# Performance work log

Hardware: AMD Instinct MI355X
Metric: run time of the kernel (lower is better)

The kernel has to match this reference:

```python
import jax, jax.numpy as jnp
import numpy as np

N = 100000
E = 1600000
D = 128  # embedding_dim
H = 128  # hidden_channels


def setup_inputs() -> dict:
    key = jax.random.key(0)
    ks = jax.random.split(key, 8)
    x = jax.random.normal(ks[0], (N, D), dtype=jnp.float32)
    edge_index = jax.random.randint(ks[1], (2, E), 0, N, dtype=jnp.int64)
    s = 1.0 / np.sqrt(D)
    W1l = jax.random.uniform(ks[2], (H, D), minval=-s, maxval=s, dtype=jnp.float32)
    W1r = jax.random.uniform(ks[3], (H, D), minval=-s, maxval=s, dtype=jnp.float32)
    b1 = jnp.zeros((H,), dtype=jnp.float32)
    s2 = 1.0 / np.sqrt(H)
    W2l = jax.random.uniform(ks[4], (H, H), minval=-s2, maxval=s2, dtype=jnp.float32)
    W2r = jax.random.uniform(ks[5], (H, H), minval=-s2, maxval=s2, dtype=jnp.float32)
    b2 = jnp.zeros((H,), dtype=jnp.float32)
    return {"x": x, "edge_index": edge_index, "W1l": W1l, "b1": b1, "W1r": W1r,
            "W2l": W2l, "b2": b2, "W2r": W2r}


def _sage_conv(h, src, dst, Wl, b, Wr, n_nodes):
    # mean aggregation of source-node features onto target nodes
    msg = h[src]                                             # [E, F] gather
    agg = jax.ops.segment_sum(msg, dst, num_segments=n_nodes)  # [N, F]
    deg = jax.ops.segment_sum(jnp.ones((src.shape[0],), h.dtype), dst,
                              num_segments=n_nodes)
    mean = agg / jnp.maximum(deg, 1.0)[:, None]
    return mean @ Wl.T + b + h @ Wr.T                        # lin_l(agg) + lin_r(x)


def reference(x, edge_index, W1l, b1, W1r, W2l, b2, W2r):
    src, dst = edge_index[0], edge_index[1]
    n = x.shape[0]
    x1 = jax.nn.relu(_sage_conv(x, src, dst, W1l, b1, W1r, n))
    x2 = jax.nn.relu(_sage_conv(x1, src, dst, W2l, b2, W2r, n))
    return jnp.concatenate((x1[:, :, None], x2[:, :, None]), axis=2)  # [N, H, 2]
```

## Files before the change

kernel.cpp:

```cpp
#include <hip/hip_runtime.h>

typedef unsigned char u8;
typedef unsigned short u16;
typedef unsigned int u32;
typedef unsigned long long u64;
typedef short bf16x8 __attribute__((ext_vector_type(8)));
typedef float f32x4 __attribute__((ext_vector_type(4)));
typedef float f32x2 __attribute__((ext_vector_type(2)));

#define NSB 32
#define MAXW 26
#define CAPL 513
#define CAPW 3072
#define CAPQ 768
#define G1 512
#define CH2 16

static __device__ __forceinline__ float relu(float v) { return v > 0.f ? v : 0.f; }

static __device__ __forceinline__ u16 f2bf(float f) {
  u32 u = __float_as_uint(f);
  u32 r = (u + 0x7FFF + ((u >> 16) & 1)) >> 16;
  return (u16)r;
}
static __device__ __forceinline__ u32 pack2(float a, float b) {
  return (u32)f2bf(a) | ((u32)f2bf(b) << 16);
}
static __device__ __forceinline__ float bflo(u32 u) { return __uint_as_float(u << 16); }
static __device__ __forceinline__ float bfhi(u32 u) { return __uint_as_float(u & 0xFFFF0000u); }

__global__ __launch_bounds__(256) void k_prep(
    const float* __restrict__ w1l, const float* __restrict__ w1r,
    const float* __restrict__ w2l, const float* __restrict__ w2r,
    u16* __restrict__ bfrag) {
  int i = blockIdx.x * 256 + threadIdx.x;
  int e = i & 7;
  int lane = (i >> 3) & 63;
  int jb = (i >> 9) & 7;
  int ks = (i >> 12) & 7;
  int m = i >> 15;
  int k = ks * 32 + (lane >> 4) * 8 + e;
  int j = jb * 16 + (lane & 15);
  const float* wl = m ? w2l : w1l;
  const float* wr = m ? w2r : w1r;
  float v = (k < 128) ? wl[j * 128 + k] : wr[j * 128 + (k - 128)];
  bfrag[i] = f2bf(v);
}

__global__ __launch_bounds__(256) void k_f2b(const float* __restrict__ x,
                                             u16* __restrict__ xb,
                                             u8* __restrict__ x8, int total8) {
  int i = blockIdx.x * 256 + threadIdx.x;
  if (i >= total8) return;
  const float4* xp = (const float4*)x;
  float4 a = xp[i * 2];
  float4 b = xp[i * 2 + 1];
  uint4 o;
  o.x = pack2(a.x, a.y);
  o.y = pack2(a.z, a.w);
  o.z = pack2(b.x, b.y);
  o.w = pack2(b.z, b.w);
  ((uint4*)xb)[i] = o;
  u32 lo = __builtin_amdgcn_cvt_pk_fp8_f32(a.x, a.y, 0u, false);
  lo = __builtin_amdgcn_cvt_pk_fp8_f32(a.z, a.w, lo, true);
  u32 hi = __builtin_amdgcn_cvt_pk_fp8_f32(b.x, b.y, 0u, false);
  hi = __builtin_amdgcn_cvt_pk_fp8_f32(b.z, b.w, hi, true);
  uint2 q = {lo, hi};
  ((uint2*)x8)[i] = q;
}

__global__ __launch_bounds__(256) void k_hist1(const int* __restrict__ dst,
                                               int* __restrict__ Hist1,
                                               int e, u32 magic, int perBlock) {
  __shared__ int h[NSB];
  int tid = threadIdx.x;
  if (tid < NSB) h[tid] = 0;
  __syncthreads();
  int start = blockIdx.x * perBlock;
  int end = min(start + perBlock, e);
  for (int i = start + tid; i < end; i += 256) {
    int d = dst[i];
    int sb = (int)(((u64)(u32)d * magic) >> 32);
    atomicAdd(&h[sb], 1);
  }
  __syncthreads();
  if (tid < NSB) Hist1[blockIdx.x * NSB + tid] = h[tid];
}

__global__ __launch_bounds__(256) void k_offs1(const int* __restrict__ Hist1,
                                               int* __restrict__ Off1,
                                               int* __restrict__ binBase1,
                                               int* __restrict__ binCnt1) {
  __shared__ int tot[NSB], base[NSB];
  int tid = threadIdx.x, lane = tid & 63, wave = tid >> 6;
  for (int b = wave * 8; b < wave * 8 + 8; ++b) {
    int run = 0;
    for (int s = 0; s < G1; s += 64) {
      int v = Hist1[(s + lane) * NSB + b];
      int sum = v;
#pragma unroll
      for (int o = 1; o < 64; o <<= 1) sum += __shfl_xor(sum, o, 64);
      run += sum;
    }
    if (lane == 0) tot[b] = run;
  }
  __syncthreads();
  if (tid == 0) {
    int r = 0;
    for (int b = 0; b < NSB; ++b) {
      base[b] = r;
      binBase1[b] = r;
      binCnt1[b] = tot[b];
      r += tot[b];
    }
  }
  __syncthreads();
  for (int b = wave * 8; b < wave * 8 + 8; ++b) {
    int run = base[b];
    for (int s = 0; s < G1; s += 64) {
      int v = Hist1[(s + lane) * NSB + b];
      int incl = v;
#pragma unroll
      for (int o = 1; o < 64; o <<= 1) {
        int t = __shfl_up(incl, o, 64);
        if (lane >= o) incl += t;
      }
      Off1[(s + lane) * NSB + b] = run + incl - v;
      run += __shfl(incl, 63, 64);
    }
  }
}

__global__ __launch_bounds__(256) void k_scatA(const int* __restrict__ src,
                                               const int* __restrict__ dst,
                                               const int* __restrict__ Off1,
                                               u32* __restrict__ gbinA,
                                               int e, int sbn, u32 magic, int perBlock) {
  __shared__ u32 lbuf[NSB * CAPL];
  __shared__ int lcnt[NSB], myOff[NSB];
  int tid = threadIdx.x, lane = tid & 63, wave = tid >> 6;
  if (tid < NSB) {
    lcnt[tid] = 0;
    myOff[tid] = Off1[blockIdx.x * NSB + tid];
  }
  __syncthreads();
  int start = blockIdx.x * perBlock;
  int end = min(start + perBlock, e);
  for (int base = start; base < end; base += 2048) {
    int bend = min(base + 2048, end);
    for (int i = base + tid; i < bend; i += 256) {
      int d = dst[i];
      int s = src[i];
      int sb = (int)(((u64)(u32)d * magic) >> 32);
      int dl = d - sb * sbn;
      u32 w = (u32)s | ((u32)dl << 17);
      int pos = atomicAdd(&lcnt[sb], 1);
      if (pos < CAPL) lbuf[sb * CAPL + pos] = w;
      else gbinA[myOff[sb] + pos] = w;
    }
    __syncthreads();
    for (int b = wave; b < NSB; b += 4) {
      int cnt = lcnt[b];
      int staged = min(cnt, CAPL);
      int gp = myOff[b];
      for (int off = lane; off < staged; off += 64) gbinA[gp + off] = lbuf[b * CAPL + off];
      if (lane == 0) {
        myOff[b] = gp + cnt;
        lcnt[b] = 0;
      }
    }
    __syncthreads();
  }
}

__global__ __launch_bounds__(256) void k_hist2(const u32* __restrict__ gbinA,
                                               const int* __restrict__ binBase1,
                                               const int* __restrict__ binCnt1,
                                               int* __restrict__ Hist2) {
  __shared__ int h[MAXW];
  int tid = threadIdx.x;
  int sb = blockIdx.x >> 4, ch = blockIdx.x & (CH2 - 1);
  if (tid < MAXW) h[tid] = 0;
  __syncthreads();
  int b0 = binBase1[sb], cnt = binCnt1[sb];
  int per = (cnt + CH2 - 1) / CH2;
  int s = b0 + ch * per, e2 = min(s + per, b0 + cnt);
  for (int i = s + tid; i < e2; i += 256) {
    int wn = (int)(gbinA[i] >> 24);
    atomicAdd(&h[wn], 1);
  }
  __syncthreads();
  if (tid < MAXW) Hist2[blockIdx.x * MAXW + tid] = h[tid];
}

__global__ __launch_bounds__(512) void k_offs2(const int* __restrict__ Hist2,
                                               int* __restrict__ Off2,
                                               int* __restrict__ winBase,
                                               int* __restrict__ winCnt, int wins) {
  __shared__ int tot[NSB * MAXW], baseL[NSB * MAXW];
  int tid = threadIdx.x, lane = tid & 63;
  int nw = NSB * wins;
  for (int wi = tid; wi < nw; wi += 512) {
    int sb = wi / wins, wn = wi - sb * wins;
    int r = 0;
    for (int ch = 0; ch < CH2; ++ch) r += Hist2[(sb * CH2 + ch) * MAXW + wn];
    tot[wi] = r;
  }
  __syncthreads();
  if (tid < 64) {
    int run = 0;
    for (int s = 0; s < nw; s += 64) {
      int idx = s + lane;
      int v = (idx < nw) ? tot[idx] : 0;
      int incl = v;
#pragma unroll
      for (int o = 1; o < 64; o <<= 1) {
        int t = __shfl_up(incl, o, 64);
        if (lane >= o) incl += t;
      }
      if (idx < nw) {
        baseL[idx] = run + incl - v;
        winBase[idx] = run + incl - v;
        winCnt[idx] = v;
      }
      run += __shfl(incl, 63, 64);
    }
  }
  __syncthreads();
  for (int wi = tid; wi < nw; wi += 512) {
    int sb = wi / wins, wn = wi - sb * wins;
    int r = baseL[wi];
    for (int ch = 0; ch < CH2; ++ch) {
      Off2[(sb * CH2 + ch) * MAXW + wn] = r;
      r += Hist2[(sb * CH2 + ch) * MAXW + wn];
    }
  }
}

__global__ __launch_bounds__(256) void k_scatB(const u32* __restrict__ gbinA,
                                               const int* __restrict__ binBase1,
                                               const int* __restrict__ binCnt1,
                                               const int* __restrict__ Off2,
                                               u32* __restrict__ gbin2, int wins) {
  __shared__ u32 lbuf[MAXW * CAPL];
  __shared__ int lcnt[MAXW], myOff[MAXW];
  int tid = threadIdx.x, lane = tid & 63, wave = tid >> 6;
  int sb = blockIdx.x >> 4, ch = blockIdx.x & (CH2 - 1);
  if (tid < MAXW) {
    lcnt[tid] = 0;
    myOff[tid] = Off2[blockIdx.x * MAXW + tid];
  }
  __syncthreads();
  int b0 = binBase1[sb], cnt = binCnt1[sb];
  int per = (cnt + CH2 - 1) / CH2;
  int s = b0 + ch * per, e2 = min(s + per, b0 + cnt);
  for (int base = s; base < e2; base += 2048) {
    int bend = min(base + 2048, e2);
    for (int i = base + tid; i < bend; i += 256) {
      u32 w = gbinA[i];
      int wn = (int)(w >> 24);
      u32 w2 = w & 0x00FFFFFFu;
      int pos = atomicAdd(&lcnt[wn], 1);
      if (pos < CAPL) lbuf[wn * CAPL + pos] = w2;
      else gbin2[myOff[wn] + pos] = w2;
    }
    __syncthreads();
    for (int b = wave; b < wins; b += 4) {
      int c = lcnt[b];
      int staged = min(c, CAPL);
      int gp = myOff[b];
      for (int off = lane; off < staged; off += 64) gbin2[gp + off] = lbuf[b * CAPL + off];
      if (lane == 0) {
        myOff[b] = gp + c;
        lcnt[b] = 0;
      }
    }
    __syncthreads();
  }
}

__global__ __launch_bounds__(256) void k_sort3(const u32* __restrict__ gbin2,
                                               const int* __restrict__ winBase,
                                               const int* __restrict__ winCnt,
                                               u32* __restrict__ gbin3,
                                               int* __restrict__ winOffs) {
  __shared__ int cnt[128], offs[128], cur[128];
  int widx = blockIdx.x, tid = threadIdx.x;
  int wstart = winBase[widx];
  int wcnt = min(winCnt[widx], CAPW);
  if (tid < 128) cnt[tid] = 0;
  __syncthreads();
  for (int i = tid; i < wcnt; i += 256) atomicAdd(&cnt[gbin2[wstart + i] >> 17], 1);
  __syncthreads();
  if (tid < 64) {
    int lane = tid;
    int c0 = cnt[lane * 2], c1 = cnt[lane * 2 + 1];
    int p = c0 + c1, incl = p;
#pragma unroll
    for (int o = 1; o < 64; o <<= 1) {
      int t = __shfl_up(incl, o, 64);
      if (lane >= o) incl += t;
    }
    offs[lane * 2] = incl - p;
    offs[lane * 2 + 1] = incl - c1;
  }
  __syncthreads();
  if (tid < 128) {
    cur[tid] = offs[tid];
    winOffs[(size_t)widx * 128 + tid] = offs[tid];
  }
  __syncthreads();
  for (int i = tid; i < wcnt; i += 256) {
    u32 w = gbin2[wstart + i];
    int pos = atomicAdd(&cur[w >> 17], 1);
    gbin3[wstart + pos] = w & 0x1FFFFu;
  }
}

__global__ __launch_bounds__(256, 8) void k_agg(
    const u8* __restrict__ h8,
    const u32* __restrict__ gbin3,
    const int* __restrict__ winBase, const int* __restrict__ winCnt,
    const int* __restrict__ winOffs, u32* __restrict__ mean,
    int n, int sbn, int wins) {
  __shared__ u32 elist[CAPQ];
  __shared__ int offs[33];
  int tid = threadIdx.x, lane = tid & 63, wid = tid >> 6;
  int widx = blockIdx.x >> 2, quarter = blockIdx.x & 3;
  int sb = widx / wins, win = widx - sb * wins;
  int winNodeBase = sb * sbn + win * 128;
  int rowsTot = min(min(128, sbn - win * 128), n - winNodeBase);
  int rowsQ = min(max(rowsTot - quarter * 32, 0), 32);
  int nodeBase = winNodeBase + quarter * 32;
  int wstart = winBase[widx];
  int wcnt = min(winCnt[widx], CAPW);
  if (tid <= 32) {
    int r = quarter * 32 + tid;
    offs[tid] = (r >= 128) ? wcnt : min(winOffs[(size_t)widx * 128 + r], wcnt);
  }
  __syncthreads();
  int s0 = offs[0];
  int cnt = min(offs[32] - s0, CAPQ);
  for (int i = tid; i < cnt; i += 256) elist[i] = gbin3[wstart + s0 + i];
  __syncthreads();

  int grp = lane >> 4, l16 = lane & 15;
  const uint2* hp = (const uint2*)h8 + l16;
#pragma unroll 1
  for (int rr = wid * 8; rr < wid * 8 + 8; ++rr) {
    int s = offs[rr] - s0;
    int e = min(offs[rr + 1] - s0, cnt);
    int c = e - s;
    float a0 = 0.f, a1 = 0.f, a2 = 0.f, a3 = 0.f;
    float a4 = 0.f, a5 = 0.f, a6 = 0.f, a7 = 0.f;
    for (int t = s + grp; t < e; t += 4) {
      u32 idx = elist[t];
      uint2 v = hp[(size_t)idx * 16];
      f32x2 f0 = __builtin_amdgcn_cvt_pk_f32_fp8(v.x, false);
      f32x2 f1 = __builtin_amdgcn_cvt_pk_f32_fp8(v.x, true);
      f32x2 f2 = __builtin_amdgcn_cvt_pk_f32_fp8(v.y, false);
      f32x2 f3 = __builtin_amdgcn_cvt_pk_f32_fp8(v.y, true);
      a0 += f0.x; a1 += f0.y; a2 += f1.x; a3 += f1.y;
      a4 += f2.x; a5 += f2.y; a6 += f3.x; a7 += f3.y;
    }
#pragma unroll
    for (int m = 16; m <= 32; m <<= 1) {
      a0 += __shfl_xor(a0, m, 64);
      a1 += __shfl_xor(a1, m, 64);
      a2 += __shfl_xor(a2, m, 64);
      a3 += __shfl_xor(a3, m, 64);
      a4 += __shfl_xor(a4, m, 64);
      a5 += __shfl_xor(a5, m, 64);
      a6 += __shfl_xor(a6, m, 64);
      a7 += __shfl_xor(a7, m, 64);
    }
    if (grp == 0 && rr < rowsQ) {
      float inv = 1.f / (float)(c > 0 ? c : 1);
      uint4 o;
      o.x = pack2(a0 * inv, a1 * inv);
      o.y = pack2(a2 * inv, a3 * inv);
      o.z = pack2(a4 * inv, a5 * inv);
      o.w = pack2(a6 * inv, a7 * inv);
      *(uint4*)(mean + (size_t)(nodeBase + rr) * 64 + l16 * 4) = o;
    }
  }
}

template <int MODE>
__global__ __launch_bounds__(512) void k_gemm(
    const u32* __restrict__ Am, const u32* __restrict__ Ax,
    const u16* __restrict__ Bfrag, const float* __restrict__ bias,
    u16* __restrict__ x1out, u8* __restrict__ x8out,
    float* __restrict__ out, int n) {
  __shared__ u16 lA[128 * 256];

  int tid = threadIdx.x, lane = tid & 63, wid = tid >> 6;
  int l15 = lane & 15, lhi = lane >> 4;
  int wr = wid >> 1, wc = wid & 1;
  int r0 = blockIdx.x * 128;

#pragma unroll
  for (int it = 0; it < 8; ++it) {
    int i = tid + it * 512;
    int row = i >> 5, c = i & 31;
    int gr = r0 + row;
    uint4 v = {0u, 0u, 0u, 0u};
    if (gr < n)
      v = (c < 16) ? ((const uint4*)(Am + (size_t)gr * 64))[c]
                   : ((const uint4*)(Ax + (size_t)gr * 64))[c - 16];
    int byteoff = (row * 512 + c * 16) ^ ((row & 7) << 4);
    *(uint4*)((char*)lA + byteoff) = v;
  }

  float bs[4];
#pragma unroll
  for (int nj = 0; nj < 4; ++nj) bs[nj] = bias[wc * 64 + nj * 16 + l15];

  __syncthreads();

  f32x4 acc[2][4];
#pragma unroll
  for (int mi = 0; mi < 2; ++mi)
#pragma unroll
    for (int nj = 0; nj < 4; ++nj) acc[mi][nj] = (f32x4){0.f, 0.f, 0.f, 0.f};

#pragma unroll
  for (int ks = 0; ks < 8; ++ks) {
    bf16x8 af[2], bfr[4];
#pragma unroll
    for (int mi = 0; mi < 2; ++mi) {
      int row = wr * 32 + mi * 16 + l15;
      int byteoff = (row * 512 + ks * 64 + lhi * 16) ^ ((row & 7) << 4);
      af[mi] = *(const bf16x8*)((const char*)lA + byteoff);
    }
#pragma unroll
    for (int nj = 0; nj < 4; ++nj) {
      int jb = wc * 4 + nj;
      bfr[nj] = *(const bf16x8*)(Bfrag + ((ks * 8 + jb) * 64 + lane) * 8);
    }
#pragma unroll
    for (int mi = 0; mi < 2; ++mi)
#pragma unroll
      for (int nj = 0; nj < 4; ++nj)
        acc[mi][nj] = __builtin_amdgcn_mfma_f32_16x16x32_bf16(af[mi], bfr[nj],
                                                              acc[mi][nj], 0, 0, 0);
  }

#pragma unroll
  for (int mi = 0; mi < 2; ++mi) {
#pragma unroll
    for (int r = 0; r < 4; ++r) {
      int rloc = wr * 32 + mi * 16 + lhi * 4 + r;
      int row = r0 + rloc;
      if (row < n) {
#pragma unroll
        for (int nj = 0; nj < 4; ++nj) {
          int col = wc * 64 + nj * 16 + l15;
          float v = relu(acc[mi][nj][r] + bs[nj]);
          if (MODE == 0) {
            x1out[(size_t)row * 128 + col] = f2bf(v);
            u32 pk = __builtin_amdgcn_cvt_pk_fp8_f32(v, v, 0u, false);
            x8out[(size_t)row * 128 + col] = (u8)(pk & 0xFF);
          } else {
            int xoff = (rloc * 512 + 256 + col * 2) ^ ((rloc & 7) << 4);
            u16 x1u = *(const u16*)((const char*)lA + xoff);
            float2 o = {__uint_as_float((u32)x1u << 16), v};
            *(float2*)&out[((size_t)row * 128 + col) * 2] = o;
          }
        }
      }
    }
  }
}

extern "C" void kernel_launch(void* const* d_in, const int* in_sizes, int n_in,
                              void* d_out, int out_size, void* d_ws, size_t ws_size,
                              hipStream_t stream) {
  const float* x = (const float*)d_in[0];
  const int* ei = (const int*)d_in[1];
  const float* w1l = (const float*)d_in[2];
  const float* b1 = (const float*)d_in[3];
  const float* w1r = (const float*)d_in[4];
  const float* w2l = (const float*)d_in[5];
  const float* b2 = (const float*)d_in[6];
  const float* w2r = (const float*)d_in[7];
  float* out = (float*)d_out;

  int n = in_sizes[0] / 128;
  int e = in_sizes[1] / 2;
  const int* src = ei;
  const int* dst = ei + e;

  int sbn = (n + NSB - 1) / NSB;
  int wins = (sbn + 127) / 128;
  u32 magic = (u32)((0x100000000ULL + sbn - 1) / (u64)sbn);

  char* ws = (char*)d_ws;
  size_t off = 0;
  auto alloc = [&](size_t bytes) {
    void* p = ws + off;
    off += (bytes + 255) & ~(size_t)255;
    return p;
  };
  u16* bfrag = (u16*)alloc(65536 * sizeof(u16));
  int* Hist1 = (int*)alloc((size_t)G1 * NSB * 4);
  int* Off1 = (int*)alloc((size_t)G1 * NSB * 4);
  int* binBase1 = (int*)alloc(NSB * 4);
  int* binCnt1 = (int*)alloc(NSB * 4);
  int* Hist2 = (int*)alloc((size_t)NSB * CH2 * MAXW * 4);
  int* Off2 = (int*)alloc((size_t)NSB * CH2 * MAXW * 4);
  int* winBase = (int*)alloc((size_t)NSB * wins * 4);
  int* winCnt = (int*)alloc((size_t)NSB * wins * 4);
  int* winOffs = (int*)alloc((size_t)NSB * wins * 128 * 4);
  u32* gbinA = (u32*)alloc((size_t)e * 4 + 256);
  u32* gbin2 = (u32*)alloc((size_t)e * 4 + 256);
  u16* xb = (u16*)alloc((size_t)n * 128 * sizeof(u16));
  u16* x1b = (u16*)alloc((size_t)n * 128 * sizeof(u16));
  u16* meanb = (u16*)alloc((size_t)n * 128 * sizeof(u16));
  u8* x8 = (u8*)alloc((size_t)n * 128);
  u8* x18 = (u8*)alloc((size_t)n * 128);
  u32* gbin3 = gbinA;
  (void)ws_size;
  (void)n_in;
  (void)out_size;

  int perBlock = (e + G1 - 1) / G1;

  k_prep<<<256, 256, 0, stream>>>(w1l, w1r, w2l, w2r, bfrag);
  k_f2b<<<(n * 128 / 8 + 255) / 256, 256, 0, stream>>>(x, xb, x8, n * 128 / 8);

  k_hist1<<<G1, 256, 0, stream>>>(dst, Hist1, e, magic, perBlock);
  k_offs1<<<1, 256, 0, stream>>>(Hist1, Off1, binBase1, binCnt1);
  k_scatA<<<G1, 256, 0, stream>>>(src, dst, Off1, gbinA, e, sbn, magic, perBlock);
  k_hist2<<<NSB * CH2, 256, 0, stream>>>(gbinA, binBase1, binCnt1, Hist2);
  k_offs2<<<1, 512, 0, stream>>>(Hist2, Off2, winBase, winCnt, wins);
  k_scatB<<<NSB * CH2, 256, 0, stream>>>(gbinA, binBase1, binCnt1, Off2, gbin2, wins);
  int gW = NSB * wins;
  k_sort3<<<gW, 256, 0, stream>>>(gbin2, winBase, winCnt, gbin3, winOffs);

  int gGemm = (n + 127) / 128;
  k_agg<<<gW * 4, 256, 0, stream>>>(x8, gbin3, winBase, winCnt, winOffs,
                                    (u32*)meanb, n, sbn, wins);
  k_gemm<0><<<gGemm, 512, 0, stream>>>((const u32*)meanb, (const u32*)xb, bfrag, b1,
                                       x1b, x18, nullptr, n);
  k_agg<<<gW * 4, 256, 0, stream>>>(x18, gbin3, winBase, winCnt, winOffs,
                                    (u32*)meanb, n, sbn, wins);
  k_gemm<1><<<gGemm, 512, 0, stream>>>((const u32*)meanb, (const u32*)x1b,
                                       bfrag + 32768, b2, nullptr, nullptr, out, n);
}
```

Measured before the change: 265.3 us.

## Merge prep, convert and histogram kernels; unroll fp8 gather with packed accumulators

Fuses the weight-fragment prep, the fp32-to-bf16/fp8 conversion and the first destination histogram into one launch, with each block picking its role from its block index. This removes two kernel launches and lets the three independent stages overlap on the device. The aggregation inner loop is also unrolled four ways with independent gathers in flight and packed f32x2 accumulators, to raise memory-level parallelism on the random row gathers. The price is higher register pressure in the aggregation kernel and a larger mixed-role grid in the fused stage.

```diff
diff --git a/kernel.cpp b/kernel.cpp
--- a/kernel.cpp
+++ b/kernel.cpp
@@ -26,65 +26,64 @@
 static __device__ __forceinline__ u32 pack2(float a, float b) {
   return (u32)f2bf(a) | ((u32)f2bf(b) << 16);
 }
-static __device__ __forceinline__ float bflo(u32 u) { return __uint_as_float(u << 16); }
-static __device__ __forceinline__ float bfhi(u32 u) { return __uint_as_float(u & 0xFFFF0000u); }
-
-__global__ __launch_bounds__(256) void k_prep(
+
+__global__ __launch_bounds__(256) void k_stage(
     const float* __restrict__ w1l, const float* __restrict__ w1r,
     const float* __restrict__ w2l, const float* __restrict__ w2r,
-    u16* __restrict__ bfrag) {
-  int i = blockIdx.x * 256 + threadIdx.x;
-  int e = i & 7;
-  int lane = (i >> 3) & 63;
-  int jb = (i >> 9) & 7;
-  int ks = (i >> 12) & 7;
-  int m = i >> 15;
-  int k = ks * 32 + (lane >> 4) * 8 + e;
-  int j = jb * 16 + (lane & 15);
-  const float* wl = m ? w2l : w1l;
-  const float* wr = m ? w2r : w1r;
-  float v = (k < 128) ? wl[j * 128 + k] : wr[j * 128 + (k - 128)];
-  bfrag[i] = f2bf(v);
-}
-
-__global__ __launch_bounds__(256) void k_f2b(const float* __restrict__ x,
-                                             u16* __restrict__ xb,
-                                             u8* __restrict__ x8, int total8) {
-  int i = blockIdx.x * 256 + threadIdx.x;
-  if (i >= total8) return;
-  const float4* xp = (const float4*)x;
-  float4 a = xp[i * 2];
-  float4 b = xp[i * 2 + 1];
-  uint4 o;
-  o.x = pack2(a.x, a.y);
-  o.y = pack2(a.z, a.w);
-  o.z = pack2(b.x, b.y);
-  o.w = pack2(b.z, b.w);
-  ((uint4*)xb)[i] = o;
-  u32 lo = __builtin_amdgcn_cvt_pk_fp8_f32(a.x, a.y, 0u, false);
-  lo = __builtin_amdgcn_cvt_pk_fp8_f32(a.z, a.w, lo, true);
-  u32 hi = __builtin_amdgcn_cvt_pk_fp8_f32(b.x, b.y, 0u, false);
-  hi = __builtin_amdgcn_cvt_pk_fp8_f32(b.z, b.w, hi, true);
-  uint2 q = {lo, hi};
-  ((uint2*)x8)[i] = q;
-}
-
-__global__ __launch_bounds__(256) void k_hist1(const int* __restrict__ dst,
-                                               int* __restrict__ Hist1,
-                                               int e, u32 magic, int perBlock) {
+    u16* __restrict__ bfrag,
+    const float* __restrict__ x, u16* __restrict__ xb, u8* __restrict__ x8,
+    int total8,
+    const int* __restrict__ dst, int* __restrict__ Hist1,
+    int e, u32 magic, int perBlock, int gPrep, int gF2b) {
   __shared__ int h[NSB];
   int tid = threadIdx.x;
-  if (tid < NSB) h[tid] = 0;
-  __syncthreads();
-  int start = blockIdx.x * perBlock;
-  int end = min(start + perBlock, e);
-  for (int i = start + tid; i < end; i += 256) {
-    int d = dst[i];
-    int sb = (int)(((u64)(u32)d * magic) >> 32);
-    atomicAdd(&h[sb], 1);
-  }
-  __syncthreads();
-  if (tid < NSB) Hist1[blockIdx.x * NSB + tid] = h[tid];
+  int b = blockIdx.x;
+  if (b < gPrep) {
+    int i = b * 256 + tid;
+    int ee = i & 7;
+    int lane = (i >> 3) & 63;
+    int jb = (i >> 9) & 7;
+    int ks = (i >> 12) & 7;
+    int m = i >> 15;
+    int k = ks * 32 + (lane >> 4) * 8 + ee;
+    int j = jb * 16 + (lane & 15);
+    const float* wl = m ? w2l : w1l;
+    const float* wr = m ? w2r : w1r;
+    float v = (k < 128) ? wl[j * 128 + k] : wr[j * 128 + (k - 128)];
+    bfrag[i] = f2bf(v);
+  } else if (b < gPrep + gF2b) {
+    int i = (b - gPrep) * 256 + tid;
+    if (i < total8) {
+      const float4* xp = (const float4*)x;
+      float4 a = xp[i * 2];
+      float4 bb = xp[i * 2 + 1];
+      uint4 o;
+      o.x = pack2(a.x, a.y);
+      o.y = pack2(a.z, a.w);
+      o.z = pack2(bb.x, bb.y);
+      o.w = pack2(bb.z, bb.w);
+      ((uint4*)xb)[i] = o;
+      u32 lo = __builtin_amdgcn_cvt_pk_fp8_f32(a.x, a.y, 0u, false);
+      lo = __builtin_amdgcn_cvt_pk_fp8_f32(a.z, a.w, lo, true);
+      u32 hi = __builtin_amdgcn_cvt_pk_fp8_f32(bb.x, bb.y, 0u, false);
+      hi = __builtin_amdgcn_cvt_pk_fp8_f32(bb.z, bb.w, hi, true);
+      uint2 q = {lo, hi};
+      ((uint2*)x8)[i] = q;
+    }
+  } else {
+    int hb = b - gPrep - gF2b;
+    if (tid < NSB) h[tid] = 0;
+    __syncthreads();
+    int start = hb * perBlock;
+    int end = min(start + perBlock, e);
+    for (int i = start + tid; i < end; i += 256) {
+      int d = dst[i];
+      int sb = (int)(((u64)(u32)d * magic) >> 32);
+      atomicAdd(&h[sb], 1);
+    }
+    __syncthreads();
+    if (tid < NSB) Hist1[hb * NSB + tid] = h[tid];
+  }
 }
 
 __global__ __launch_bounds__(256) void k_offs1(const int* __restrict__ Hist1,
@@ -351,18 +350,46 @@
     int s = offs[rr] - s0;
     int e = min(offs[rr + 1] - s0, cnt);
     int c = e - s;
-    float a0 = 0.f, a1 = 0.f, a2 = 0.f, a3 = 0.f;
-    float a4 = 0.f, a5 = 0.f, a6 = 0.f, a7 = 0.f;
-    for (int t = s + grp; t < e; t += 4) {
-      u32 idx = elist[t];
-      uint2 v = hp[(size_t)idx * 16];
-      f32x2 f0 = __builtin_amdgcn_cvt_pk_f32_fp8(v.x, false);
-      f32x2 f1 = __builtin_amdgcn_cvt_pk_f32_fp8(v.x, true);
-      f32x2 f2 = __builtin_amdgcn_cvt_pk_f32_fp8(v.y, false);
-      f32x2 f3 = __builtin_amdgcn_cvt_pk_f32_fp8(v.y, true);
-      a0 += f0.x; a1 += f0.y; a2 += f1.x; a3 += f1.y;
-      a4 += f2.x; a5 += f2.y; a6 += f3.x; a7 += f3.y;
-    }
+    f32x2 A0 = {0.f, 0.f}, A1 = {0.f, 0.f}, A2 = {0.f, 0.f}, A3 = {0.f, 0.f};
+    int t = s + grp;
+    int cg = e - t;
+    int nit = (cg > 0) ? ((cg + 3) >> 2) : 0;
+    int nq = nit >> 2, rem = nit & 3;
+    for (int q = 0; q < nq; ++q) {
+      u32 i0 = elist[t], i1 = elist[t + 4], i2 = elist[t + 8], i3 = elist[t + 12];
+      uint2 va = hp[(size_t)i0 * 16];
+      uint2 vb = hp[(size_t)i1 * 16];
+      uint2 vc = hp[(size_t)i2 * 16];
+      uint2 vd = hp[(size_t)i3 * 16];
+      A0 += __builtin_amdgcn_cvt_pk_f32_fp8(va.x, false);
+      A1 += __builtin_amdgcn_cvt_pk_f32_fp8(va.x, true);
+      A2 += __builtin_amdgcn_cvt_pk_f32_fp8(va.y, false);
+      A3 += __builtin_amdgcn_cvt_pk_f32_fp8(va.y, true);
+      A0 += __builtin_amdgcn_cvt_pk_f32_fp8(vb.x, false);
+      A1 += __builtin_amdgcn_cvt_pk_f32_fp8(vb.x, true);
+      A2 += __builtin_amdgcn_cvt_pk_f32_fp8(vb.y, false);
+      A3 += __builtin_amdgcn_cvt_pk_f32_fp8(vb.y, true);
+      A0 += __builtin_amdgcn_cvt_pk_f32_fp8(vc.x, false);
+      A1 += __builtin_amdgcn_cvt_pk_f32_fp8(vc.x, true);
+      A2 += __builtin_amdgcn_cvt_pk_f32_fp8(vc.y, false);
+      A3 += __builtin_amdgcn_cvt_pk_f32_fp8(vc.y, true);
+      A0 += __builtin_amdgcn_cvt_pk_f32_fp8(vd.x, false);
+      A1 += __builtin_amdgcn_cvt_pk_f32_fp8(vd.x, true);
+      A2 += __builtin_amdgcn_cvt_pk_f32_fp8(vd.y, false);
+      A3 += __builtin_amdgcn_cvt_pk_f32_fp8(vd.y, true);
+      t += 16;
+    }
+    for (int r2 = 0; r2 < rem; ++r2) {
+      u32 i0 = elist[t];
+      uint2 va = hp[(size_t)i0 * 16];
+      A0 += __builtin_amdgcn_cvt_pk_f32_fp8(va.x, false);
+      A1 += __builtin_amdgcn_cvt_pk_f32_fp8(va.x, true);
+      A2 += __builtin_amdgcn_cvt_pk_f32_fp8(va.y, false);
+      A3 += __builtin_amdgcn_cvt_pk_f32_fp8(va.y, true);
+      t += 4;
+    }
+    float a0 = A0.x, a1 = A0.y, a2 = A1.x, a3 = A1.y;
+    float a4 = A2.x, a5 = A2.y, a6 = A3.x, a7 = A3.y;
 #pragma unroll
     for (int m = 16; m <= 32; m <<= 1) {
       a0 += __shfl_xor(a0, m, 64);
@@ -525,11 +552,13 @@
   (void)out_size;
 
   int perBlock = (e + G1 - 1) / G1;
-
-  k_prep<<<256, 256, 0, stream>>>(w1l, w1r, w2l, w2r, bfrag);
-  k_f2b<<<(n * 128 / 8 + 255) / 256, 256, 0, stream>>>(x, xb, x8, n * 128 / 8);
-
-  k_hist1<<<G1, 256, 0, stream>>>(dst, Hist1, e, magic, perBlock);
+  int total8 = n * 128 / 8;
+  int gPrep = 256;
+  int gF2b = (total8 + 255) / 256;
+
+  k_stage<<<gPrep + gF2b + G1, 256, 0, stream>>>(
+      w1l, w1r, w2l, w2r, bfrag, x, xb, x8, total8, dst, Hist1, e, magic,
+      perBlock, gPrep, gF2b);
   k_offs1<<<1, 256, 0, stream>>>(Hist1, Off1, binBase1, binCnt1);
   k_scatA<<<G1, 256, 0, stream>>>(src, dst, Off1, gbinA, e, sbn, magic, perBlock);
   k_hist2<<<NSB * CH2, 256, 0, stream>>>(gbinA, binBase1, binCnt1, Hist2);
```

New measurement: 242.2 us. 1.1x faster.
